# Kernel optimization log

Measured on AMD Instinct MI355X. Metric: run time of the kernel, lower is better.

## Reference

```python
import jax, jax.numpy as jnp
import numpy as np


def setup_inputs() -> dict:
    key = jax.random.key(0)
    ks = jax.random.split(key, 6)
    B, C_in, C_out, H, W = 4, 256, 128, 64, 64
    return {
        "p": jax.random.normal(ks[0], (B, C_in, H, W), dtype=jnp.float32),
        "b": jax.random.normal(ks[1], (B, C_in, H, W), dtype=jnp.float32),
        "Wq": jax.random.normal(ks[2], (C_out, C_in), dtype=jnp.float32) * 0.05,
        "bq": jax.random.normal(ks[3], (C_out,), dtype=jnp.float32) * 0.05,
        "Wk": jax.random.normal(ks[4], (C_out, C_in), dtype=jnp.float32) * 0.05,
        "bk": jax.random.normal(ks[5], (C_out,), dtype=jnp.float32) * 0.05,
    }


def reference(p, b, Wq, bq, Wk, bk):
    # p, b: [B, C, H, W]; 1x1 convs are per-pixel GEMMs over channels.
    B, C, H, W = p.shape
    N = H * W
    p_flat = p.reshape(B, C, N)  # [B, C, N]
    b_flat = b.reshape(B, C, N)  # [B, C, N]
    # query = Conv1x1(p) -> [B, O, N] -> permuted to [B, N, O]
    q = jnp.einsum("bcn,oc->bno", p_flat, Wq) + bq  # [B, N, O]
    # key = Conv1x1(b) -> [B, O, N]
    k = jnp.einsum("bcn,oc->bon", b_flat, Wk) + bk[:, None]  # [B, O, N]
    energy = jnp.einsum("bno,bom->bnm", q, k)  # [B, N, N]
    attention = jax.nn.softmax(energy, axis=-1)
    # value = b flattened, attention applied over spatial tokens
    out = jnp.einsum("bnm,bcm->bcn", attention, b_flat)  # [B, C, N]
    return out.reshape(B, C, H, W)
```

## Files before the change

### kernel.cpp

```cpp
#include <hip/hip_runtime.h>
#include <stdint.h>


#define B_ 4
#define C_ 256
#define O_ 128
#define N_ 4096

#define AP 72
#define PFP 72

typedef float v4f __attribute__((ext_vector_type(4)));
typedef short v8s __attribute__((ext_vector_type(8)));
typedef _Float16 v8h __attribute__((ext_vector_type(8)));
typedef uint32_t u32;
typedef unsigned short u16;

__device__ __forceinline__ u16 bf16_rne(float f) {
  u32 u = __builtin_bit_cast(u32, f);
  u += 0x7fffu + ((u >> 16) & 1u);
  return (u16)(u >> 16);
}
__device__ __forceinline__ float bf16_f(u16 s) {
  u32 u = ((u32)s) << 16;
  return __builtin_bit_cast(float, u);
}
__device__ __forceinline__ u16 f16_rne(float f) {
  _Float16 h = (_Float16)f;
  return __builtin_bit_cast(u16, h);
}
__device__ __forceinline__ float f16_f(u16 s) {
  return (float)__builtin_bit_cast(_Float16, s);
}
__device__ __forceinline__ v4f mfma16(v8s a, v8s b, v4f c) {
  return __builtin_amdgcn_mfma_f32_16x16x32_bf16(a, b, c, 0, 0, 0);
}
__device__ __forceinline__ v4f mfma16h(v8h a, v8h b, v4f c) {
  return __builtin_amdgcn_mfma_f32_16x16x32_f16(a, b, c, 0, 0, 0);
}
__device__ __forceinline__ void gl16(const u16* g, u16* l) {
  __builtin_amdgcn_global_load_lds(
      (const __attribute__((address_space(1))) u32*)g,
      (__attribute__((address_space(3))) u32*)l, 16, 0, 0);
}
template <int CTRL>
__device__ __forceinline__ float dppadd(float x) {
  int yi = __builtin_amdgcn_update_dpp(0, __builtin_bit_cast(int, x), CTRL,
                                       0xf, 0xf, true);
  return x + __builtin_bit_cast(float, yi);
}
__device__ __forceinline__ float sum16(float x) {
  x = dppadd<0xB1>(x);
  x = dppadd<0x4E>(x);
  x = dppadd<0x141>(x);
  x = dppadd<0x140>(x);
  return x;
}

__global__ __launch_bounds__(256) void k_proj(
    const float* __restrict__ Xp, const float* __restrict__ Wq,
    const float* __restrict__ bq, const float* __restrict__ Xb,
    const float* __restrict__ Wk, const float* __restrict__ bk,
    u16* __restrict__ Qh, u16* __restrict__ Ql, u16* __restrict__ Kh,
    u16* __restrict__ Vbf) {
  __shared__ __align__(16) short ah[64 * AP];
  __shared__ __align__(16) short al[64 * AP];
  __shared__ __align__(16) short wh[128 * AP];
  __shared__ __align__(16) short wl[128 * AP];
  const int tid = threadIdx.x;
  const int inst = blockIdx.x >> 8;
  const float* X = inst ? Xb : Xp;
  const float* W = inst ? Wk : Wq;
  const float* bias = inst ? bk : bq;
  const int b = (blockIdx.x >> 6) & 3;
  const int n0 = (blockIdx.x & 63) << 6;
  const int w = tid >> 6, lane = tid & 63, l15 = lane & 15, quad = lane >> 4;
  v4f acc[8];
#pragma unroll
  for (int t = 0; t < 8; t++) acc[t] = (v4f){0.f, 0.f, 0.f, 0.f};

  for (int c0 = 0; c0 < C_; c0 += 64) {
    __syncthreads();
    {
      const int c = tid >> 2, nch = (tid & 3) << 4;
      const float* s = X + ((size_t)(b * C_ + c0 + c)) * N_ + n0 + nch;
      float4 f0 = ((const float4*)s)[0], f1 = ((const float4*)s)[1],
             f2 = ((const float4*)s)[2], f3 = ((const float4*)s)[3];
      float v[16] = {f0.x, f0.y, f0.z, f0.w, f1.x, f1.y, f1.z, f1.w,
                     f2.x, f2.y, f2.z, f2.w, f3.x, f3.y, f3.z, f3.w};
      u16 hh[16];
#pragma unroll
      for (int j = 0; j < 16; j++) {
        u16 h = bf16_rne(v[j]);
        u16 l = bf16_rne(v[j] - bf16_f(h));
        hh[j] = h;
        ah[(nch + j) * AP + c] = (short)h;
        al[(nch + j) * AP + c] = (short)l;
      }
      if (inst) {
        u32 pk[8];
#pragma unroll
        for (int jj = 0; jj < 8; jj++)
          pk[jj] = (u32)hh[2 * jj] | ((u32)hh[2 * jj + 1] << 16);
        u16* vd = Vbf + ((size_t)(b * C_ + c0 + c)) * N_ + n0 + nch;
        ((uint4*)vd)[0] = make_uint4(pk[0], pk[1], pk[2], pk[3]);
        ((uint4*)vd)[1] = make_uint4(pk[4], pk[5], pk[6], pk[7]);
      }
    }
    {
      const int o = tid >> 1, cch = (tid & 1) << 5;
      const float* s = W + (size_t)o * C_ + c0 + cch;
#pragma unroll
      for (int jj = 0; jj < 8; jj++) {
        float4 f = ((const float4*)s)[jj];
        float v[4] = {f.x, f.y, f.z, f.w};
#pragma unroll
        for (int j = 0; j < 4; j++) {
          u16 h = bf16_rne(v[j]);
          u16 l = bf16_rne(v[j] - bf16_f(h));
          wh[o * AP + cch + jj * 4 + j] = (short)h;
          wl[o * AP + cch + jj * 4 + j] = (short)l;
        }
      }
    }
    __syncthreads();
#pragma unroll
    for (int s = 0; s < 2; s++) {
      v8s a_h = *(const v8s*)&ah[(16 * w + l15) * AP + 32 * s + 8 * quad];
      v8s a_l = *(const v8s*)&al[(16 * w + l15) * AP + 32 * s + 8 * quad];
#pragma unroll
      for (int to = 0; to < 8; to++) {
        v8s b_h = *(const v8s*)&wh[(16 * to + l15) * AP + 32 * s + 8 * quad];
        v8s b_l = *(const v8s*)&wl[(16 * to + l15) * AP + 32 * s + 8 * quad];
        acc[to] = mfma16(a_h, b_h, acc[to]);
        acc[to] = mfma16(a_h, b_l, acc[to]);
        acc[to] = mfma16(a_l, b_h, acc[to]);
      }
    }
  }
#pragma unroll
  for (int to = 0; to < 8; to++) {
    const int o = 16 * to + l15;
    const float bv = bias[o];
#pragma unroll
    for (int r = 0; r < 4; r++) {
      const int n = n0 + 16 * w + 4 * quad + r;
      float v = acc[to][r] + bv;
      const size_t idx = (size_t)(b * N_ + n) * O_ + o;
      if (!inst) {
        u16 h = f16_rne(v);
        Qh[idx] = h;
        Ql[idx] = f16_rne(v - f16_f(h));
      } else {
        Kh[idx] = f16_rne(v);
      }
    }
  }
}

__global__ __launch_bounds__(512, 4) void k_flash(
    const u16* __restrict__ Qh, const u16* __restrict__ Ql,
    const u16* __restrict__ Khp, const u16* __restrict__ Vbf,
    u16* __restrict__ Opart, float* __restrict__ lpart) {
  __shared__ __align__(16) short smem[20992];
  short* Pt = smem + 16384;

  const int tid = threadIdx.x;
  const int w = tid >> 6, lane = tid & 63, l15 = lane & 15, quad = lane >> 4;
  const int wr = w & 3, wh2 = w >> 2;
  const int xcd = blockIdx.x & 7;
  const int b = xcd >> 1, h = xcd & 1;
  const int qt = blockIdx.x >> 3;
  const int n0 = qt << 6;
  const int tok0 = h << 11;
  const int og = (b << 7) + (qt << 1) + h;

  const u16* khb = Khp + (size_t)b * N_ * O_;
  const u16* vb = Vbf + (size_t)b * C_ * N_;

  v8h qh[4], ql[4];
  {
    const u16* qrh = Qh + (size_t)(b * N_ + n0 + 16 * wr + l15) * O_;
    const u16* qrl = Ql + (size_t)(b * N_ + n0 + 16 * wr + l15) * O_;
#pragma unroll
    for (int s = 0; s < 4; s++) {
      qh[s] = *(const v8h*)(qrh + 32 * s + 8 * quad);
      ql[s] = *(const v8h*)(qrl + 32 * s + 8 * quad);
    }
  }

  v4f oacc[8];
#pragma unroll
  for (int t = 0; t < 8; t++) oacc[t] = (v4f){0.f, 0.f, 0.f, 0.f};
  float lstate[4] = {0.f, 0.f, 0.f, 0.f};

  auto stageK = [&](int mtn, int bi) {
    const int m0n = tok0 + (mtn << 6);
    short* kd = smem + bi * 8192;
#pragma unroll
    for (int i = 0; i < 2; i++) {
      const int R = 8 * w + 4 * i;
      const int rl = R + (lane >> 4);
      const int cg = (lane & 15) ^ (rl & 15);
      gl16(khb + ((size_t)(m0n + rl) << 7) + (cg << 3), (u16*)(kd + (R << 7)));
    }
  };

  stageK(0, 0);

  const u16* vrow = vb + (size_t)(32 * w + l15) * N_ + (quad << 3);

#pragma unroll 1
  for (int mt = 0; mt < 32; mt++) {
    const int pr = mt & 1;
    const int m0 = tok0 + (mt << 6);
    __syncthreads();

    v8s vfr[2][2];
#pragma unroll
    for (int cg = 0; cg < 2; cg++)
#pragma unroll
      for (int s = 0; s < 2; s++)
        vfr[cg][s] =
            *(const v8s*)(vrow + (size_t)(cg << 4) * N_ + m0 + (s << 5));

    if (mt + 1 < 32) stageK(mt + 1, 1 - pr);
    const short* kc = smem + pr * 8192;

    v4f eh[2], el[2];
#pragma unroll
    for (int t = 0; t < 2; t++) {
      eh[t] = (v4f){0.f, 0.f, 0.f, 0.f};
      el[t] = (v4f){0.f, 0.f, 0.f, 0.f};
    }
#pragma unroll
    for (int s = 0; s < 4; s++) {
#pragma unroll
      for (int t = 0; t < 2; t++) {
        const int row = (wh2 << 5) + (t << 4) + l15;
        const int off = (row << 7) + (((4 * s + quad) ^ l15) << 3);
        const v8h kf = *(const v8h*)&kc[off];
        eh[t] = mfma16h(qh[s], kf, eh[t]);
        el[t] = mfma16h(ql[s], kf, el[t]);
      }
    }

#pragma unroll
    for (int r = 0; r < 4; r++) {
      float p0 = __expf(eh[0][r] + el[0][r]);
      float p1 = __expf(eh[1][r] + el[1][r]);
      lstate[r] += sum16(p0 + p1);
      const int prow = ((wr << 4) + 4 * quad + r) * PFP + (wh2 << 5);
      Pt[prow + l15] = (short)bf16_rne(p0);
      Pt[prow + 16 + l15] = (short)bf16_rne(p1);
    }
    __builtin_amdgcn_s_waitcnt(0xC07F);
    asm volatile("s_barrier" ::: "memory");

#pragma unroll
    for (int s = 0; s < 2; s++) {
      v8s af[4];
#pragma unroll
      for (int rw = 0; rw < 4; rw++)
        af[rw] =
            *(const v8s*)&Pt[((rw << 4) + l15) * PFP + (s << 5) + (quad << 3)];
#pragma unroll
      for (int cg = 0; cg < 2; cg++)
#pragma unroll
        for (int rw = 0; rw < 4; rw++)
          oacc[rw * 2 + cg] = mfma16(af[rw], vfr[cg][s], oacc[rw * 2 + cg]);
    }
  }

  __syncthreads();
  u16* outx = (u16*)smem;
#pragma unroll
  for (int rw = 0; rw < 4; rw++)
#pragma unroll
    for (int cg = 0; cg < 2; cg++) {
      const int ch = (w << 5) + (cg << 4) + l15;
      const v4f o = oacc[rw * 2 + cg];
      u32* q = (u32*)outx;
      const int base = ch * 36 + (rw << 3) + (quad << 1);
      q[base] = (u32)bf16_rne(o[0]) | ((u32)bf16_rne(o[1]) << 16);
      q[base + 1] = (u32)bf16_rne(o[2]) | ((u32)bf16_rne(o[3]) << 16);
    }
  if (l15 == 0) {
#pragma unroll
    for (int r = 0; r < 4; r++)
      lpart[(size_t)og * 128 + (wh2 << 6) + (wr << 4) + 4 * quad + r] =
          lstate[r];
  }
  __syncthreads();
  {
    u16* od = Opart + (size_t)og * 16384;
    const int cr = tid >> 3, col = (tid & 7) << 3;
#pragma unroll
    for (int it = 0; it < 4; it++) {
      const int c = cr + 64 * it;
      *(uint4*)(od + c * 64 + col) = *(const uint4*)&outx[c * 72 + col];
    }
  }
}

__global__ __launch_bounds__(256) void k_merge(const u16* __restrict__ Opart,
                                               const float* __restrict__ lpart,
                                               float* __restrict__ out) {
  const int idx = blockIdx.x * 256 + threadIdx.x;
  const int e4 = idx << 2;
  const int b = e4 >> 20;
  const int c = (e4 >> 12) & 255;
  const int n = e4 & 4095;
  const int qt = n >> 6, row = n & 63;
  const int g2 = (b << 7) + (qt << 1);
  const u16* q0 = Opart + (size_t)g2 * 16384 + c * 64 + row;
  ushort4 a0 = *(const ushort4*)q0;
  ushort4 a1 = *(const ushort4*)(q0 + 16384);
  const float* lb = lpart + (size_t)g2 * 128 + row;
  float4 l0 = *(const float4*)lb;
  float4 l1 = *(const float4*)(lb + 64);
  float4 l2 = *(const float4*)(lb + 128);
  float4 l3 = *(const float4*)(lb + 192);
  float4 o;
  o.x = (bf16_f(a0.x) + bf16_f(a1.x)) / (l0.x + l1.x + l2.x + l3.x);
  o.y = (bf16_f(a0.y) + bf16_f(a1.y)) / (l0.y + l1.y + l2.y + l3.y);
  o.z = (bf16_f(a0.z) + bf16_f(a1.z)) / (l0.z + l1.z + l2.z + l3.z);
  o.w = (bf16_f(a0.w) + bf16_f(a1.w)) / (l0.w + l1.w + l2.w + l3.w);
  *(float4*)(out + e4) = o;
}

extern "C" void kernel_launch(void* const* d_in, const int* in_sizes, int n_in,
                              void* d_out, int out_size, void* d_ws, size_t ws_size,
                              hipStream_t stream) {
  const float* p = (const float*)d_in[0];
  const float* bb = (const float*)d_in[1];
  const float* Wq = (const float*)d_in[2];
  const float* bq = (const float*)d_in[3];
  const float* Wk = (const float*)d_in[4];
  const float* bk = (const float*)d_in[5];
  float* out = (float*)d_out;

  const size_t plane = (size_t)B_ * N_ * O_;
  u16* Qh = (u16*)d_ws;
  u16* Ql = Qh + plane;
  u16* Kh = Ql + plane;
  u16* Vbf = Kh + plane;
  u16* Opart = Vbf + 2 * plane;
  float* lpart = (float*)(Opart + (size_t)512 * 16384);

  hipLaunchKernelGGL(k_proj, dim3(512), dim3(256), 0, stream, p, Wq, bq, bb,
                     Wk, bk, Qh, Ql, Kh, Vbf);
  hipLaunchKernelGGL(k_flash, dim3(B_ * 64 * 2), dim3(512), 0, stream, Qh, Ql,
                     Kh, Vbf, Opart, lpart);
  hipLaunchKernelGGL(k_merge, dim3((B_ * C_ * N_) / (256 * 4)), dim3(256), 0,
                     stream, Opart, lpart, out);
}
```

Baseline: 193.4 us.

## Software-pipeline flash loop with double-buffered swizzled P tiles

Restructures the attention main loop so each iteration runs the QK^T MFMAs for tile mt alongside the P·V MFMAs for tile mt-1. The probability tile P is double-buffered in LDS, which removes the mid-iteration barrier between writing and reading P. P's row stride also changes from a padded 72 to 64 with an XOR swizzle to avoid bank conflicts. PV is wrapped in s_setprio. Shared memory grows from about 41 KB to 48 KB per block, which could lower occupancy, and V register fragments now stay live across the loop boundary.

```diff
diff --git a/kernel.cpp b/kernel.cpp
--- a/kernel.cpp
+++ b/kernel.cpp
@@ -8,7 +8,6 @@
 #define N_ 4096
 
 #define AP 72
-#define PFP 72
 
 typedef float v4f __attribute__((ext_vector_type(4)));
 typedef short v8s __attribute__((ext_vector_type(8)));
@@ -162,8 +161,7 @@
     const u16* __restrict__ Qh, const u16* __restrict__ Ql,
     const u16* __restrict__ Khp, const u16* __restrict__ Vbf,
     u16* __restrict__ Opart, float* __restrict__ lpart) {
-  __shared__ __align__(16) short smem[20992];
-  short* Pt = smem + 16384;
+  __shared__ __align__(16) short smem[24576];
 
   const int tid = threadIdx.x;
   const int w = tid >> 6, lane = tid & 63, l15 = lane & 15, quad = lane >> 4;
@@ -206,28 +204,8 @@
     }
   };
 
-  stageK(0, 0);
-
-  const u16* vrow = vb + (size_t)(32 * w + l15) * N_ + (quad << 3);
-
-#pragma unroll 1
-  for (int mt = 0; mt < 32; mt++) {
-    const int pr = mt & 1;
-    const int m0 = tok0 + (mt << 6);
-    __syncthreads();
-
-    v8s vfr[2][2];
-#pragma unroll
-    for (int cg = 0; cg < 2; cg++)
-#pragma unroll
-      for (int s = 0; s < 2; s++)
-        vfr[cg][s] =
-            *(const v8s*)(vrow + (size_t)(cg << 4) * N_ + m0 + (s << 5));
-
-    if (mt + 1 < 32) stageK(mt + 1, 1 - pr);
-    const short* kc = smem + pr * 8192;
-
-    v4f eh[2], el[2];
+  v4f eh[2], el[2];
+  auto doQK = [&](const short* kc) {
 #pragma unroll
     for (int t = 0; t < 2; t++) {
       eh[t] = (v4f){0.f, 0.f, 0.f, 0.f};
@@ -244,35 +222,78 @@
         el[t] = mfma16h(ql[s], kf, el[t]);
       }
     }
-
+  };
+
+  auto doSM = [&](short* Pc) {
 #pragma unroll
     for (int r = 0; r < 4; r++) {
       float p0 = __expf(eh[0][r] + el[0][r]);
       float p1 = __expf(eh[1][r] + el[1][r]);
       lstate[r] += sum16(p0 + p1);
-      const int prow = ((wr << 4) + 4 * quad + r) * PFP + (wh2 << 5);
-      Pt[prow + l15] = (short)bf16_rne(p0);
-      Pt[prow + 16 + l15] = (short)bf16_rne(p1);
-    }
-    __builtin_amdgcn_s_waitcnt(0xC07F);
-    asm volatile("s_barrier" ::: "memory");
-
+      const int row = (wr << 4) + 4 * quad + r;
+      const int sw = (row & 7) << 3;
+      const int c0 = (wh2 << 5) + l15;
+      Pc[(row << 6) + (c0 ^ sw)] = (short)bf16_rne(p0);
+      Pc[(row << 6) + ((c0 + 16) ^ sw)] = (short)bf16_rne(p1);
+    }
+  };
+
+  v8s vfr[2][2];
+  auto doPV = [&](const short* Pp) {
+    __builtin_amdgcn_s_setprio(1);
 #pragma unroll
     for (int s = 0; s < 2; s++) {
       v8s af[4];
 #pragma unroll
-      for (int rw = 0; rw < 4; rw++)
-        af[rw] =
-            *(const v8s*)&Pt[((rw << 4) + l15) * PFP + (s << 5) + (quad << 3)];
+      for (int rw = 0; rw < 4; rw++) {
+        const int row = (rw << 4) + l15;
+        const int col = ((s << 5) + (quad << 3)) ^ ((row & 7) << 3);
+        af[rw] = *(const v8s*)&Pp[(row << 6) + col];
+      }
 #pragma unroll
       for (int cg = 0; cg < 2; cg++)
 #pragma unroll
         for (int rw = 0; rw < 4; rw++)
           oacc[rw * 2 + cg] = mfma16(af[rw], vfr[cg][s], oacc[rw * 2 + cg]);
     }
-  }
-
+    __builtin_amdgcn_s_setprio(0);
+  };
+
+  const u16* vrow = vb + (size_t)(32 * w + l15) * N_ + (quad << 3);
+  auto loadV = [&](int mtn) {
+    const int m0 = tok0 + (mtn << 6);
+#pragma unroll
+    for (int cg = 0; cg < 2; cg++)
+#pragma unroll
+      for (int s = 0; s < 2; s++)
+        vfr[cg][s] =
+            *(const v8s*)(vrow + (size_t)(cg << 4) * N_ + m0 + (s << 5));
+  };
+
+  short* const P0 = smem + 16384;
+  short* const P1 = smem + 16384 + 4096;
+
+  stageK(0, 0);
   __syncthreads();
+  stageK(1, 1);
+  doQK(smem);
+  doSM(P0);
+  loadV(0);
+
+#pragma unroll 1
+  for (int mt = 1; mt < 32; mt++) {
+    const int pr = mt & 1;
+    __syncthreads();
+    if (mt + 1 < 32) stageK(mt + 1, 1 - pr);
+    doQK(smem + pr * 8192);
+    doPV(pr ? P0 : P1);
+    doSM(pr ? P1 : P0);
+    loadV(mt);
+  }
+
+  __syncthreads();
+  doPV(P1);
+
   u16* outx = (u16*)smem;
 #pragma unroll
   for (int rw = 0; rw < 4; rw++)
```

Measured after the change: 238.4 us. +23.3%, slower.

## Triple-buffer K tiles with prefetch depth two and XOR-swizzle P tile

Applied to the files above, without the earlier changes.

Moves K staging in the flash kernel from double to triple buffering, issuing async loads two tiles ahead and waiting with a partial vmcnt so one tile's load stays in flight across the barrier. The P tile drops its padded pitch for an XOR-swizzled 64-wide layout to avoid LDS bank conflicts. The row-sum shuffle reduction is deferred until after the PV MFMAs so it can overlap. LDS use grows, which may lower occupancy under the 4-blocks-per-CU launch bound.

```diff
diff --git a/kernel.cpp b/kernel.cpp
--- a/kernel.cpp
+++ b/kernel.cpp
@@ -8,7 +8,6 @@
 #define N_ 4096
 
 #define AP 72
-#define PFP 72
 
 typedef float v4f __attribute__((ext_vector_type(4)));
 typedef short v8s __attribute__((ext_vector_type(8)));
@@ -162,8 +161,8 @@
     const u16* __restrict__ Qh, const u16* __restrict__ Ql,
     const u16* __restrict__ Khp, const u16* __restrict__ Vbf,
     u16* __restrict__ Opart, float* __restrict__ lpart) {
-  __shared__ __align__(16) short smem[20992];
-  short* Pt = smem + 16384;
+  __shared__ __align__(16) short smem[28672];
+  short* const Pt = smem + 24576;
 
   const int tid = threadIdx.x;
   const int w = tid >> 6, lane = tid & 63, l15 = lane & 15, quad = lane >> 4;
@@ -206,26 +205,29 @@
     }
   };
 
-  stageK(0, 0);
-
+  v8s vfr[2][2];
   const u16* vrow = vb + (size_t)(32 * w + l15) * N_ + (quad << 3);
-
-#pragma unroll 1
-  for (int mt = 0; mt < 32; mt++) {
-    const int pr = mt & 1;
-    const int m0 = tok0 + (mt << 6);
-    __syncthreads();
-
-    v8s vfr[2][2];
+  auto loadV = [&](int mtn) {
+    const int m0 = tok0 + (mtn << 6);
 #pragma unroll
     for (int cg = 0; cg < 2; cg++)
 #pragma unroll
       for (int s = 0; s < 2; s++)
         vfr[cg][s] =
             *(const v8s*)(vrow + (size_t)(cg << 4) * N_ + m0 + (s << 5));
-
-    if (mt + 1 < 32) stageK(mt + 1, 1 - pr);
-    const short* kc = smem + pr * 8192;
+  };
+
+  stageK(0, 0);
+  stageK(1, 1);
+
+  int rb = 0, sb = 2;
+#pragma unroll 1
+  for (int mt = 0; mt < 32; mt++) {
+    __builtin_amdgcn_s_waitcnt(0x0F72);
+    asm volatile("s_barrier" ::: "memory");
+
+    loadV(mt);
+    if (mt + 2 < 32) stageK(mt + 2, sb);
 
     v4f eh[2], el[2];
 #pragma unroll
@@ -233,6 +235,7 @@
       eh[t] = (v4f){0.f, 0.f, 0.f, 0.f};
       el[t] = (v4f){0.f, 0.f, 0.f, 0.f};
     }
+    const short* kc = smem + rb * 8192;
 #pragma unroll
     for (int s = 0; s < 4; s++) {
 #pragma unroll
@@ -245,14 +248,17 @@
       }
     }
 
+    float pp[4];
 #pragma unroll
     for (int r = 0; r < 4; r++) {
       float p0 = __expf(eh[0][r] + el[0][r]);
       float p1 = __expf(eh[1][r] + el[1][r]);
-      lstate[r] += sum16(p0 + p1);
-      const int prow = ((wr << 4) + 4 * quad + r) * PFP + (wh2 << 5);
-      Pt[prow + l15] = (short)bf16_rne(p0);
-      Pt[prow + 16 + l15] = (short)bf16_rne(p1);
+      const int row = (wr << 4) + 4 * quad + r;
+      const int sw = (row & 7) << 3;
+      const int c0 = (wh2 << 5) + l15;
+      Pt[(row << 6) + (c0 ^ sw)] = (short)bf16_rne(p0);
+      Pt[(row << 6) + ((c0 + 16) ^ sw)] = (short)bf16_rne(p1);
+      pp[r] = p0 + p1;
     }
     __builtin_amdgcn_s_waitcnt(0xC07F);
     asm volatile("s_barrier" ::: "memory");
@@ -261,15 +267,22 @@
     for (int s = 0; s < 2; s++) {
       v8s af[4];
 #pragma unroll
-      for (int rw = 0; rw < 4; rw++)
-        af[rw] =
-            *(const v8s*)&Pt[((rw << 4) + l15) * PFP + (s << 5) + (quad << 3)];
+      for (int rw = 0; rw < 4; rw++) {
+        const int row = (rw << 4) + l15;
+        const int col = ((s << 5) + (quad << 3)) ^ ((row & 7) << 3);
+        af[rw] = *(const v8s*)&Pt[(row << 6) + col];
+      }
 #pragma unroll
       for (int cg = 0; cg < 2; cg++)
 #pragma unroll
         for (int rw = 0; rw < 4; rw++)
           oacc[rw * 2 + cg] = mfma16(af[rw], vfr[cg][s], oacc[rw * 2 + cg]);
     }
+#pragma unroll
+    for (int r = 0; r < 4; r++) lstate[r] += sum16(pp[r]);
+
+    rb = (rb == 2) ? 0 : rb + 1;
+    sb = (sb == 2) ? 0 : sb + 1;
   }
 
   __syncthreads();
```

Measured after the change: 224.8 us. 1.16x slower.
